# Kernel tuning notes

Hardware: AMD Instinct MI355X
Metric: run time of the kernel (lower is better)

## Reference

```python
import jax, jax.numpy as jnp
import numpy as np

N = 100_000      # nodes
E = 1_600_000    # edges (avg degree 16)
IN, HID, OUT = 256, 256, 128  # in_dim, 2*out_dim, out_dim
BN_EPS = 1e-5


def setup_inputs() -> dict:
    key = jax.random.key(0)
    ks = jax.random.split(key, 8)
    x = jax.random.normal(ks[0], (N, IN), jnp.float32)
    edge_index = jax.random.randint(ks[1], (2, E), 0, N, dtype=jnp.int64)
    # GCNConv weights (glorot-ish scaling) + biases
    W1 = jax.random.normal(ks[2], (IN, HID), jnp.float32) * (1.0 / np.sqrt(IN))
    b1 = jnp.zeros((HID,), jnp.float32)
    W2 = jax.random.normal(ks[3], (HID, OUT), jnp.float32) * (1.0 / np.sqrt(HID))
    b2 = jnp.zeros((OUT,), jnp.float32)
    # BatchNorm1d affine params
    gamma = jnp.ones((HID,), jnp.float32)
    beta = jnp.zeros((HID,), jnp.float32)
    # PReLU single learnable slope (torch default 0.25)
    a = jnp.full((1,), 0.25, jnp.float32)
    return {"x": x, "edge_index": edge_index, "W1": W1, "b1": b1,
            "W2": W2, "b2": b2, "gamma": gamma, "beta": beta, "a": a}


def gcn_layer(x, W, b, src, dst):
    """GCNConv: h = D^-1/2 (A + I) D^-1/2 (x @ W) + b, self-loop weight 1."""
    h = x @ W                                           # [N, F]
    deg = jnp.zeros((N,), h.dtype).at[dst].add(1.0) + 1.0  # +1 self-loop
    dinv = jax.lax.rsqrt(deg)                           # [N]
    norm = dinv[src] * dinv[dst]                        # [E]
    agg = jnp.zeros_like(h).at[dst].add(h[src] * norm[:, None])
    agg = agg + h * (dinv * dinv)[:, None]              # self-loop term
    return agg + b


def reference(x, edge_index, W1, b1, W2, b2, gamma, beta, a):
    src, dst = edge_index[0], edge_index[1]
    h = gcn_layer(x, W1, b1, src, dst)                  # [N, HID]
    # BatchNorm1d (training mode: batch statistics, biased var)
    mean = jnp.mean(h, axis=0)
    var = jnp.var(h, axis=0)
    h = (h - mean) * jax.lax.rsqrt(var + BN_EPS) * gamma + beta
    # PReLU with single shared slope
    h = jnp.where(h > 0, h, a * h)
    return gcn_layer(h, W2, b2, src, dst)               # [N, OUT]
```

## Files before the change

kernel.cpp:

```cpp
#include <hip/hip_runtime.h>
#include <hip/hip_bf16.h>
#include <stdint.h>

#define IN_DIM 256

typedef __attribute__((ext_vector_type(8))) short short8;
typedef __attribute__((ext_vector_type(4))) float f32x4;

__device__ __forceinline__ float bf2f(unsigned short u){
  return __uint_as_float(((unsigned int)u) << 16);
}
__device__ __forceinline__ unsigned short f2bf(float f){
  unsigned int u = __float_as_uint(f);
  u = u + 0x7FFFu + ((u >> 16) & 1u);
  return (unsigned short)(u >> 16);
}

__global__ void k_detect(const void* ei, long long E, int N, int* flag){
  __shared__ int bad;
  if (threadIdx.x == 0) bad = 0;
  __syncthreads();
  const long long* p = (const long long*)ei;
  long long stride = E / 1024; if (stride < 1) stride = 1;
  for (int i = threadIdx.x; i < 1024; i += blockDim.x){
    long long idx = (long long)i * stride;
    if (idx >= E) break;
    long long v = p[idx];
    if (v < 0 || v >= (long long)N) atomicOr(&bad, 1);
  }
  __syncthreads();
  if (threadIdx.x == 0) flag[0] = bad ? 0 : 1;
}

__device__ __forceinline__ int edge_at(const void* ei, long long i, int f64){
  if (f64) return (int)((const long long*)ei)[i];
  return ((const int*)ei)[i];
}

__global__ void k_hist(const void* ei, long long E, const int* flag, int* cnt){
  long long e = (long long)blockIdx.x * blockDim.x + threadIdx.x;
  if (e < E){
    int f = flag[0];
    int d = edge_at(ei, E + e, f);
    atomicAdd(&cnt[d], 1);
  }
}

__global__ void k_scan1(const int* cnt, int* rs, int* bsum, float* dinv, int* fill, int N){
  __shared__ int sh[1024];
  int i = blockIdx.x * 1024 + threadIdx.x;
  int v = (i < N) ? cnt[i] : 0;
  sh[threadIdx.x] = v;
  __syncthreads();
  for (int o = 1; o < 1024; o <<= 1){
    int x = (threadIdx.x >= o) ? sh[threadIdx.x - o] : 0;
    __syncthreads();
    sh[threadIdx.x] += x;
    __syncthreads();
  }
  if (i < N){
    rs[i] = sh[threadIdx.x] - v;
    dinv[i] = rsqrtf((float)v + 1.0f);
    fill[i] = 0;
  }
  if (threadIdx.x == 1023) bsum[blockIdx.x] = sh[1023];
}

__global__ void k_scan2(const int* bsum, int* boff, int nb, int* rs, int N,
                        float* sums, float* sqs){
  __shared__ int sh[128];
  int t = threadIdx.x;
  int v = (t < nb) ? bsum[t] : 0;
  sh[t] = v;
  __syncthreads();
  for (int o = 1; o < 128; o <<= 1){
    int x = (t >= o) ? sh[t - o] : 0;
    __syncthreads();
    sh[t] += x;
    __syncthreads();
  }
  boff[t] = sh[t] - v;
  if (t == 127) rs[N] = sh[127];
  sums[t] = 0.f; sums[t + 128] = 0.f;
  sqs[t]  = 0.f; sqs[t + 128]  = 0.f;
}

__global__ void k_scan3(int* rs, const int* boff, int N){
  int i = blockIdx.x * 1024 + threadIdx.x;
  if (i < N) rs[i] += boff[blockIdx.x];
}

__global__ void k_scatter(const void* ei, long long E, const int* flag, const int* rs,
                          int* fill, int* csrc){
  long long e = (long long)blockIdx.x * blockDim.x + threadIdx.x;
  if (e < E){
    int f = flag[0];
    int s = edge_at(ei, e, f);
    int d = edge_at(ei, E + e, f);
    int pos = atomicAdd(&fill[d], 1);
    csrc[rs[d] + pos] = s;
  }
}

__global__ void k_prep(const float* __restrict__ x, ushort* __restrict__ xb,
                       const float* __restrict__ W1, ushort* __restrict__ W1t,
                       const float* __restrict__ W2, ushort* __restrict__ W2t,
                       int N, int NP){
  int idx = blockIdx.x * 256 + threadIdx.x;
  int nxq = NP * 64;
  if (idx < nxq){
    int row = idx >> 6, q = idx & 63;
    ushort4 o = {0, 0, 0, 0};
    if (row < N){
      float4 v = ((const float4*)x)[(size_t)row * 64 + q];
      o.x = f2bf(v.x); o.y = f2bf(v.y); o.z = f2bf(v.z); o.w = f2bf(v.w);
    }
    ((ushort4*)xb)[idx] = o;
  } else {
    int j = idx - nxq;
    if (j < 256 * 256){
      int n = j >> 8, k = j & 255;
      W1t[j] = f2bf(W1[(size_t)k * 256 + n]);
    } else {
      j -= 65536;
      if (j < 128 * 256){
        int n = j >> 8, k = j & 255;
        W2t[j] = f2bf(W2[(size_t)k * 128 + n]);
      }
    }
  }
}

__global__ __launch_bounds__(256) void k_gemm(const ushort* __restrict__ A,
                                              const ushort* __restrict__ Bt,
                                              ushort* __restrict__ C,
                                              const float* __restrict__ dinv,
                                              int N, int Nc){
  __shared__ ushort As[128 * 64];
  __shared__ ushort Bs[128 * 64];
  const int tid = threadIdx.x;
  const int wave = tid >> 6, lane = tid & 63;
  const long long row0 = (long long)blockIdx.x * 128;
  const int col0 = blockIdx.y * 128;
  const int lr = lane >> 3, lc = lane & 7;
  const int mrow = ((wave & 1) << 6) + (lane & 15);
  const int ncol = ((wave >> 1) << 6) + (lane & 15);

  f32x4 acc[4][4];
  #pragma unroll
  for (int i = 0; i < 4; ++i)
    #pragma unroll
    for (int j = 0; j < 4; ++j)
      acc[i][j] = (f32x4){0.f, 0.f, 0.f, 0.f};

  const ushort* gA = A + (row0 + wave * 32 + lr) * 256 + lc * 8;
  const ushort* gB = Bt + ((long long)(col0 + wave * 32 + lr)) * 256 + lc * 8;
  ushort* lA = As + wave * 2048;
  ushort* lB = Bs + wave * 2048;

  #pragma unroll
  for (int kt = 0; kt < 4; ++kt){
    #pragma unroll
    for (int i = 0; i < 4; ++i){
      __builtin_amdgcn_global_load_lds(
          (const __attribute__((address_space(1))) void*)(gA + kt * 64 + i * 8 * 256),
          (__attribute__((address_space(3))) void*)(lA + i * 512), 16, 0, 0);
      __builtin_amdgcn_global_load_lds(
          (const __attribute__((address_space(1))) void*)(gB + kt * 64 + i * 8 * 256),
          (__attribute__((address_space(3))) void*)(lB + i * 512), 16, 0, 0);
    }
    __syncthreads();
    #pragma unroll
    for (int ks = 0; ks < 2; ++ks){
      const int kb = ks * 32 + ((lane >> 4) << 3);
      short8 af[4], bfv[4];
      #pragma unroll
      for (int i = 0; i < 4; ++i) af[i] = *(const short8*)(As + (mrow + i * 16) * 64 + kb);
      #pragma unroll
      for (int j = 0; j < 4; ++j) bfv[j] = *(const short8*)(Bs + (ncol + j * 16) * 64 + kb);
      #pragma unroll
      for (int i = 0; i < 4; ++i)
        #pragma unroll
        for (int j = 0; j < 4; ++j)
          acc[i][j] = __builtin_amdgcn_mfma_f32_16x16x32_bf16(af[i], bfv[j], acc[i][j], 0, 0, 0);
    }
    __syncthreads();
  }

  const int rbase = ((wave & 1) << 6) + ((lane >> 4) << 2);
  const int cb = col0 + ((wave >> 1) << 6) + (lane & 15);
  #pragma unroll
  for (int i = 0; i < 4; ++i)
    #pragma unroll
    for (int r = 0; r < 4; ++r){
      long long row = row0 + rbase + i * 16 + r;
      float sc = (row < N) ? dinv[row] : 0.f;
      #pragma unroll
      for (int j = 0; j < 4; ++j)
        C[row * Nc + cb + j * 16] = f2bf(sc * acc[i][j][r]);
    }
}

__global__ __launch_bounds__(64) void k_agg1(const ushort* __restrict__ hs, const int* __restrict__ rs,
    const int* __restrict__ csrc, const float* __restrict__ dinv, const float* __restrict__ b1,
    ushort* __restrict__ h1){
  int n = blockIdx.x;
  int t = threadIdx.x;
  const ushort4* hv = (const ushort4*)hs;
  ushort4 sv = hv[(size_t)n * 64 + t];
  float a0 = bf2f(sv.x), a1 = bf2f(sv.y), a2 = bf2f(sv.z), a3 = bf2f(sv.w);
  int e = rs[n], end = rs[n + 1];
  for (; e + 4 <= end; e += 4){
    int s0 = csrc[e], s1 = csrc[e + 1], s2 = csrc[e + 2], s3 = csrc[e + 3];
    ushort4 v0 = hv[(size_t)s0 * 64 + t];
    ushort4 v1 = hv[(size_t)s1 * 64 + t];
    ushort4 v2 = hv[(size_t)s2 * 64 + t];
    ushort4 v3 = hv[(size_t)s3 * 64 + t];
    a0 += bf2f(v0.x) + bf2f(v1.x) + bf2f(v2.x) + bf2f(v3.x);
    a1 += bf2f(v0.y) + bf2f(v1.y) + bf2f(v2.y) + bf2f(v3.y);
    a2 += bf2f(v0.z) + bf2f(v1.z) + bf2f(v2.z) + bf2f(v3.z);
    a3 += bf2f(v0.w) + bf2f(v1.w) + bf2f(v2.w) + bf2f(v3.w);
  }
  for (; e < end; ++e){
    int s = csrc[e];
    ushort4 v = hv[(size_t)s * 64 + t];
    a0 += bf2f(v.x); a1 += bf2f(v.y); a2 += bf2f(v.z); a3 += bf2f(v.w);
  }
  float dn = dinv[n];
  float4 bb = ((const float4*)b1)[t];
  ushort4 o;
  o.x = f2bf(dn * a0 + bb.x);
  o.y = f2bf(dn * a1 + bb.y);
  o.z = f2bf(dn * a2 + bb.z);
  o.w = f2bf(dn * a3 + bb.w);
  ((ushort4*)h1)[(size_t)n * 64 + t] = o;
}

__global__ __launch_bounds__(64) void k_agg2(const ushort* __restrict__ h2, const int* __restrict__ rs,
    const int* __restrict__ csrc, const float* __restrict__ dinv, const float* __restrict__ b2,
    float* __restrict__ out){
  int n = blockIdx.x;
  int t = threadIdx.x;
  const uint* hv = (const uint*)h2;
  uint sv = hv[(size_t)n * 64 + t];
  float a0 = bf2f((unsigned short)(sv & 0xFFFF));
  float a1 = bf2f((unsigned short)(sv >> 16));
  int e = rs[n], end = rs[n + 1];
  for (; e + 4 <= end; e += 4){
    int s0 = csrc[e], s1 = csrc[e + 1], s2 = csrc[e + 2], s3 = csrc[e + 3];
    uint v0 = hv[(size_t)s0 * 64 + t];
    uint v1 = hv[(size_t)s1 * 64 + t];
    uint v2 = hv[(size_t)s2 * 64 + t];
    uint v3 = hv[(size_t)s3 * 64 + t];
    a0 += bf2f((unsigned short)(v0 & 0xFFFF)) + bf2f((unsigned short)(v1 & 0xFFFF))
        + bf2f((unsigned short)(v2 & 0xFFFF)) + bf2f((unsigned short)(v3 & 0xFFFF));
    a1 += bf2f((unsigned short)(v0 >> 16)) + bf2f((unsigned short)(v1 >> 16))
        + bf2f((unsigned short)(v2 >> 16)) + bf2f((unsigned short)(v3 >> 16));
  }
  for (; e < end; ++e){
    int s = csrc[e];
    uint v = hv[(size_t)s * 64 + t];
    a0 += bf2f((unsigned short)(v & 0xFFFF));
    a1 += bf2f((unsigned short)(v >> 16));
  }
  float dn = dinv[n];
  float2 bb = ((const float2*)b2)[t];
  float2 r; r.x = dn * a0 + bb.x; r.y = dn * a1 + bb.y;
  ((float2*)out)[(size_t)n * 64 + t] = r;
}

__global__ void k_bnstats(const ushort* __restrict__ h1, float* __restrict__ sums,
                          float* __restrict__ sqs, int N){
  int cp = threadIdx.x & 127, ro = threadIdx.x >> 7;
  const uint* hv = (const uint*)h1;
  float s0 = 0.f, s1 = 0.f, q0 = 0.f, q1 = 0.f;
  for (int r = blockIdx.x * 2 + ro; r < N; r += gridDim.x * 2){
    uint v = hv[(size_t)r * 128 + cp];
    float x0 = bf2f((unsigned short)(v & 0xFFFF));
    float x1 = bf2f((unsigned short)(v >> 16));
    s0 += x0; q0 += x0 * x0;
    s1 += x1; q1 += x1 * x1;
  }
  atomicAdd(&sums[2 * cp],     s0);
  atomicAdd(&sums[2 * cp + 1], s1);
  atomicAdd(&sqs[2 * cp],      q0);
  atomicAdd(&sqs[2 * cp + 1],  q1);
}

__global__ void k_prelu(const ushort* __restrict__ h1, const float* __restrict__ sums,
                        const float* __restrict__ sqs, const float* __restrict__ gamma,
                        const float* __restrict__ beta, const float* __restrict__ aP,
                        ushort* __restrict__ P, int N, int NP){
  int idx = blockIdx.x * 256 + threadIdx.x;
  int row = idx >> 7, cp = idx & 127;
  if (row >= NP) return;
  uint o = 0;
  if (row < N){
    int c0 = 2 * cp;
    float inv = 1.0f / (float)N;
    float m0 = sums[c0] * inv,     m1 = sums[c0 + 1] * inv;
    float v0 = sqs[c0] * inv - m0 * m0, v1 = sqs[c0 + 1] * inv - m1 * m1;
    float sc0 = gamma[c0] * rsqrtf(v0 + 1e-5f);
    float sc1 = gamma[c0 + 1] * rsqrtf(v1 + 1e-5f);
    float sh0 = beta[c0] - m0 * sc0;
    float sh1 = beta[c0 + 1] - m1 * sc1;
    uint v = ((const uint*)h1)[(size_t)row * 128 + cp];
    float aa = aP[0];
    float x0 = bf2f((unsigned short)(v & 0xFFFF)) * sc0 + sh0;
    float x1 = bf2f((unsigned short)(v >> 16)) * sc1 + sh1;
    x0 = x0 > 0.f ? x0 : aa * x0;
    x1 = x1 > 0.f ? x1 : aa * x1;
    o = (uint)f2bf(x0) | ((uint)f2bf(x1) << 16);
  }
  ((uint*)P)[idx] = o;
}

extern "C" void kernel_launch(void* const* d_in, const int* in_sizes, int n_in,
                              void* d_out, int out_size, void* d_ws, size_t ws_size,
                              hipStream_t stream){
  const float* x  = (const float*)d_in[0];
  const void*  ei = d_in[1];
  const float* W1 = (const float*)d_in[2];
  const float* b1 = (const float*)d_in[3];
  const float* W2 = (const float*)d_in[4];
  const float* b2 = (const float*)d_in[5];
  const float* gm = (const float*)d_in[6];
  const float* bt = (const float*)d_in[7];
  const float* aP = (const float*)d_in[8];
  float* out = (float*)d_out;

  const int N = in_sizes[0] / IN_DIM;
  const long long E = in_sizes[1] / 2;
  const int NP = ((N + 127) / 128) * 128;

  char* w = (char*)d_ws;
  size_t off = 0;
  auto carve = [&](size_t bytes) -> char* {
    char* p = w + off;
    off += (bytes + 255) & ~(size_t)255;
    return p;
  };
  ushort* xb  = (ushort*)carve((size_t)NP * 256 * 2);
  ushort* hb  = (ushort*)carve((size_t)NP * 256 * 2);
  ushort* h1b = (ushort*)carve((size_t)NP * 256 * 2);
  ushort* W1t = (ushort*)carve(256 * 256 * 2);
  ushort* W2t = (ushort*)carve(128 * 256 * 2);
  int*   cnt  = (int*)  carve((size_t)N * 4);
  int*   rs   = (int*)  carve((size_t)(N + 1) * 4);
  int*   fill = (int*)  carve((size_t)N * 4);
  int*   csrc = (int*)  carve((size_t)E * 4);
  float* dinv = (float*)carve((size_t)N * 4);
  int*   bsum = (int*)  carve(512);
  int*   boff = (int*)  carve(512);
  float* sums = (float*)carve(1024);
  float* sqs  = (float*)carve(1024);
  int*   flag = (int*)  carve(256);

  const int NB1 = (N + 1023) / 1024;
  const int egrid = (int)((E + 255) / 256);
  const int prep_grid = (NP * 64 + 256 * 256 + 128 * 256 + 255) / 256;

  k_detect<<<1, 256, 0, stream>>>(ei, E, N, flag);
  hipMemsetAsync(cnt, 0, (size_t)N * 4, stream);
  k_prep<<<prep_grid, 256, 0, stream>>>(x, xb, W1, W1t, W2, W2t, N, NP);
  k_hist<<<egrid, 256, 0, stream>>>(ei, E, flag, cnt);
  k_scan1<<<NB1, 1024, 0, stream>>>(cnt, rs, bsum, dinv, fill, N);
  k_scan2<<<1, 128, 0, stream>>>(bsum, boff, NB1, rs, N, sums, sqs);
  k_scan3<<<NB1, 1024, 0, stream>>>(rs, boff, N);
  k_scatter<<<egrid, 256, 0, stream>>>(ei, E, flag, rs, fill, csrc);

  k_gemm<<<dim3(NP / 128, 2), 256, 0, stream>>>(xb, W1t, hb, dinv, N, 256);
  k_agg1<<<N, 64, 0, stream>>>(hb, rs, csrc, dinv, b1, h1b);
  k_bnstats<<<256, 256, 0, stream>>>(h1b, sums, sqs, N);
  k_prelu<<<(NP * 128 + 255) / 256, 256, 0, stream>>>(h1b, sums, sqs, gm, bt, aP, xb, N, NP);
  k_gemm<<<dim3(NP / 128, 1), 256, 0, stream>>>(xb, W2t, hb, dinv, N, 128);
  k_agg2<<<N, 64, 0, stream>>>(hb, rs, csrc, dinv, b2, out);
}
```

Baseline: 675.5 us.

## Use persistent wave-per-node aggregation with wave-wide index load and readlane broadcast

Both aggregation kernels switch from one 64-thread block per node to a fixed grid of 2048 blocks of 256 threads. Each wave walks nodes in a grid-stride loop. A wave loads up to 64 neighbour indices in one coalesced read, broadcasts them with readlane, and unrolls the gathers by 8 to keep more loads in flight. This removes the cost of launching 100k tiny blocks and the scalar per-edge index loads. In exchange, the fixed grid may leave load imbalance across waves when node degrees vary.

```diff
diff --git a/kernel.cpp b/kernel.cpp
--- a/kernel.cpp
+++ b/kernel.cpp
@@ -3,6 +3,7 @@
 #include <stdint.h>
 
 #define IN_DIM 256
+#define AGG_BLOCKS 2048
 
 typedef __attribute__((ext_vector_type(8))) short short8;
 typedef __attribute__((ext_vector_type(4))) float f32x4;
@@ -201,72 +202,123 @@
     }
 }
 
-__global__ __launch_bounds__(64) void k_agg1(const ushort* __restrict__ hs, const int* __restrict__ rs,
+__global__ __launch_bounds__(256) void k_agg1(const ushort* __restrict__ hs, const int* __restrict__ rs,
     const int* __restrict__ csrc, const float* __restrict__ dinv, const float* __restrict__ b1,
-    ushort* __restrict__ h1){
-  int n = blockIdx.x;
-  int t = threadIdx.x;
-  const ushort4* hv = (const ushort4*)hs;
-  ushort4 sv = hv[(size_t)n * 64 + t];
-  float a0 = bf2f(sv.x), a1 = bf2f(sv.y), a2 = bf2f(sv.z), a3 = bf2f(sv.w);
-  int e = rs[n], end = rs[n + 1];
-  for (; e + 4 <= end; e += 4){
-    int s0 = csrc[e], s1 = csrc[e + 1], s2 = csrc[e + 2], s3 = csrc[e + 3];
-    ushort4 v0 = hv[(size_t)s0 * 64 + t];
-    ushort4 v1 = hv[(size_t)s1 * 64 + t];
-    ushort4 v2 = hv[(size_t)s2 * 64 + t];
-    ushort4 v3 = hv[(size_t)s3 * 64 + t];
-    a0 += bf2f(v0.x) + bf2f(v1.x) + bf2f(v2.x) + bf2f(v3.x);
-    a1 += bf2f(v0.y) + bf2f(v1.y) + bf2f(v2.y) + bf2f(v3.y);
-    a2 += bf2f(v0.z) + bf2f(v1.z) + bf2f(v2.z) + bf2f(v3.z);
-    a3 += bf2f(v0.w) + bf2f(v1.w) + bf2f(v2.w) + bf2f(v3.w);
-  }
-  for (; e < end; ++e){
-    int s = csrc[e];
-    ushort4 v = hv[(size_t)s * 64 + t];
-    a0 += bf2f(v.x); a1 += bf2f(v.y); a2 += bf2f(v.z); a3 += bf2f(v.w);
-  }
-  float dn = dinv[n];
-  float4 bb = ((const float4*)b1)[t];
-  ushort4 o;
-  o.x = f2bf(dn * a0 + bb.x);
-  o.y = f2bf(dn * a1 + bb.y);
-  o.z = f2bf(dn * a2 + bb.z);
-  o.w = f2bf(dn * a3 + bb.w);
-  ((ushort4*)h1)[(size_t)n * 64 + t] = o;
-}
-
-__global__ __launch_bounds__(64) void k_agg2(const ushort* __restrict__ h2, const int* __restrict__ rs,
+    ushort* __restrict__ h1, int N){
+  const int lane = threadIdx.x & 63;
+  const int wid = (blockIdx.x * 256 + threadIdx.x) >> 6;
+  const int nw = (AGG_BLOCKS * 256) >> 6;
+  const float4 bb = ((const float4*)b1)[lane];
+
+  for (int n = wid; n < N; n += nw){
+    const ushort4* selfp = (const ushort4*)(hs + (size_t)n * 256);
+    ushort4 sv = selfp[lane];
+    float a0 = bf2f(sv.x), a1 = bf2f(sv.y), a2 = bf2f(sv.z), a3 = bf2f(sv.w);
+    int e0 = rs[n], deg = rs[n + 1] - e0;
+
+    for (int c = 0; c < deg; c += 64){
+      int chunk = deg - c; if (chunk > 64) chunk = 64;
+      int myc = 0;
+      if (lane < chunk) myc = csrc[e0 + c + lane];
+      int j = 0;
+      for (; j + 8 <= chunk; j += 8){
+        int s0 = __builtin_amdgcn_readlane(myc, j);
+        int s1 = __builtin_amdgcn_readlane(myc, j + 1);
+        int s2 = __builtin_amdgcn_readlane(myc, j + 2);
+        int s3 = __builtin_amdgcn_readlane(myc, j + 3);
+        int s4 = __builtin_amdgcn_readlane(myc, j + 4);
+        int s5 = __builtin_amdgcn_readlane(myc, j + 5);
+        int s6 = __builtin_amdgcn_readlane(myc, j + 6);
+        int s7 = __builtin_amdgcn_readlane(myc, j + 7);
+        ushort4 v0 = ((const ushort4*)(hs + (size_t)s0 * 256))[lane];
+        ushort4 v1 = ((const ushort4*)(hs + (size_t)s1 * 256))[lane];
+        ushort4 v2 = ((const ushort4*)(hs + (size_t)s2 * 256))[lane];
+        ushort4 v3 = ((const ushort4*)(hs + (size_t)s3 * 256))[lane];
+        ushort4 v4 = ((const ushort4*)(hs + (size_t)s4 * 256))[lane];
+        ushort4 v5 = ((const ushort4*)(hs + (size_t)s5 * 256))[lane];
+        ushort4 v6 = ((const ushort4*)(hs + (size_t)s6 * 256))[lane];
+        ushort4 v7 = ((const ushort4*)(hs + (size_t)s7 * 256))[lane];
+        a0 += ((bf2f(v0.x) + bf2f(v1.x)) + (bf2f(v2.x) + bf2f(v3.x)))
+            + ((bf2f(v4.x) + bf2f(v5.x)) + (bf2f(v6.x) + bf2f(v7.x)));
+        a1 += ((bf2f(v0.y) + bf2f(v1.y)) + (bf2f(v2.y) + bf2f(v3.y)))
+            + ((bf2f(v4.y) + bf2f(v5.y)) + (bf2f(v6.y) + bf2f(v7.y)));
+        a2 += ((bf2f(v0.z) + bf2f(v1.z)) + (bf2f(v2.z) + bf2f(v3.z)))
+            + ((bf2f(v4.z) + bf2f(v5.z)) + (bf2f(v6.z) + bf2f(v7.z)));
+        a3 += ((bf2f(v0.w) + bf2f(v1.w)) + (bf2f(v2.w) + bf2f(v3.w)))
+            + ((bf2f(v4.w) + bf2f(v5.w)) + (bf2f(v6.w) + bf2f(v7.w)));
+      }
+      for (; j < chunk; ++j){
+        int s = __builtin_amdgcn_readlane(myc, j);
+        ushort4 v = ((const ushort4*)(hs + (size_t)s * 256))[lane];
+        a0 += bf2f(v.x); a1 += bf2f(v.y); a2 += bf2f(v.z); a3 += bf2f(v.w);
+      }
+    }
+    float dn = dinv[n];
+    ushort4 o;
+    o.x = f2bf(dn * a0 + bb.x);
+    o.y = f2bf(dn * a1 + bb.y);
+    o.z = f2bf(dn * a2 + bb.z);
+    o.w = f2bf(dn * a3 + bb.w);
+    ((ushort4*)h1)[(size_t)n * 64 + lane] = o;
+  }
+}
+
+__global__ __launch_bounds__(256) void k_agg2(const ushort* __restrict__ h2, const int* __restrict__ rs,
     const int* __restrict__ csrc, const float* __restrict__ dinv, const float* __restrict__ b2,
-    float* __restrict__ out){
-  int n = blockIdx.x;
-  int t = threadIdx.x;
-  const uint* hv = (const uint*)h2;
-  uint sv = hv[(size_t)n * 64 + t];
-  float a0 = bf2f((unsigned short)(sv & 0xFFFF));
-  float a1 = bf2f((unsigned short)(sv >> 16));
-  int e = rs[n], end = rs[n + 1];
-  for (; e + 4 <= end; e += 4){
-    int s0 = csrc[e], s1 = csrc[e + 1], s2 = csrc[e + 2], s3 = csrc[e + 3];
-    uint v0 = hv[(size_t)s0 * 64 + t];
-    uint v1 = hv[(size_t)s1 * 64 + t];
-    uint v2 = hv[(size_t)s2 * 64 + t];
-    uint v3 = hv[(size_t)s3 * 64 + t];
-    a0 += bf2f((unsigned short)(v0 & 0xFFFF)) + bf2f((unsigned short)(v1 & 0xFFFF))
-        + bf2f((unsigned short)(v2 & 0xFFFF)) + bf2f((unsigned short)(v3 & 0xFFFF));
-    a1 += bf2f((unsigned short)(v0 >> 16)) + bf2f((unsigned short)(v1 >> 16))
-        + bf2f((unsigned short)(v2 >> 16)) + bf2f((unsigned short)(v3 >> 16));
-  }
-  for (; e < end; ++e){
-    int s = csrc[e];
-    uint v = hv[(size_t)s * 64 + t];
-    a0 += bf2f((unsigned short)(v & 0xFFFF));
-    a1 += bf2f((unsigned short)(v >> 16));
-  }
-  float dn = dinv[n];
-  float2 bb = ((const float2*)b2)[t];
-  float2 r; r.x = dn * a0 + bb.x; r.y = dn * a1 + bb.y;
-  ((float2*)out)[(size_t)n * 64 + t] = r;
+    float* __restrict__ out, int N){
+  const int lane = threadIdx.x & 63;
+  const int wid = (blockIdx.x * 256 + threadIdx.x) >> 6;
+  const int nw = (AGG_BLOCKS * 256) >> 6;
+  const float2 bb = ((const float2*)b2)[lane];
+
+  for (int n = wid; n < N; n += nw){
+    uint sv = ((const uint*)(h2 + (size_t)n * 128))[lane];
+    float a0 = bf2f((unsigned short)(sv & 0xFFFF));
+    float a1 = bf2f((unsigned short)(sv >> 16));
+    int e0 = rs[n], deg = rs[n + 1] - e0;
+
+    for (int c = 0; c < deg; c += 64){
+      int chunk = deg - c; if (chunk > 64) chunk = 64;
+      int myc = 0;
+      if (lane < chunk) myc = csrc[e0 + c + lane];
+      int j = 0;
+      for (; j + 8 <= chunk; j += 8){
+        int s0 = __builtin_amdgcn_readlane(myc, j);
+        int s1 = __builtin_amdgcn_readlane(myc, j + 1);
+        int s2 = __builtin_amdgcn_readlane(myc, j + 2);
+        int s3 = __builtin_amdgcn_readlane(myc, j + 3);
+        int s4 = __builtin_amdgcn_readlane(myc, j + 4);
+        int s5 = __builtin_amdgcn_readlane(myc, j + 5);
+        int s6 = __builtin_amdgcn_readlane(myc, j + 6);
+        int s7 = __builtin_amdgcn_readlane(myc, j + 7);
+        uint v0 = ((const uint*)(h2 + (size_t)s0 * 128))[lane];
+        uint v1 = ((const uint*)(h2 + (size_t)s1 * 128))[lane];
+        uint v2 = ((const uint*)(h2 + (size_t)s2 * 128))[lane];
+        uint v3 = ((const uint*)(h2 + (size_t)s3 * 128))[lane];
+        uint v4 = ((const uint*)(h2 + (size_t)s4 * 128))[lane];
+        uint v5 = ((const uint*)(h2 + (size_t)s5 * 128))[lane];
+        uint v6 = ((const uint*)(h2 + (size_t)s6 * 128))[lane];
+        uint v7 = ((const uint*)(h2 + (size_t)s7 * 128))[lane];
+        a0 += ((bf2f((unsigned short)(v0 & 0xFFFF)) + bf2f((unsigned short)(v1 & 0xFFFF)))
+             + (bf2f((unsigned short)(v2 & 0xFFFF)) + bf2f((unsigned short)(v3 & 0xFFFF))))
+            + ((bf2f((unsigned short)(v4 & 0xFFFF)) + bf2f((unsigned short)(v5 & 0xFFFF)))
+             + (bf2f((unsigned short)(v6 & 0xFFFF)) + bf2f((unsigned short)(v7 & 0xFFFF))));
+        a1 += ((bf2f((unsigned short)(v0 >> 16)) + bf2f((unsigned short)(v1 >> 16)))
+             + (bf2f((unsigned short)(v2 >> 16)) + bf2f((unsigned short)(v3 >> 16))))
+            + ((bf2f((unsigned short)(v4 >> 16)) + bf2f((unsigned short)(v5 >> 16)))
+             + (bf2f((unsigned short)(v6 >> 16)) + bf2f((unsigned short)(v7 >> 16))));
+      }
+      for (; j < chunk; ++j){
+        int s = __builtin_amdgcn_readlane(myc, j);
+        uint v = ((const uint*)(h2 + (size_t)s * 128))[lane];
+        a0 += bf2f((unsigned short)(v & 0xFFFF));
+        a1 += bf2f((unsigned short)(v >> 16));
+      }
+    }
+    float dn = dinv[n];
+    float2 r; r.x = dn * a0 + bb.x; r.y = dn * a1 + bb.y;
+    ((float2*)out)[(size_t)n * 64 + lane] = r;
+  }
 }
 
 __global__ void k_bnstats(const ushort* __restrict__ h1, float* __restrict__ sums,
@@ -370,9 +422,9 @@
   k_scatter<<<egrid, 256, 0, stream>>>(ei, E, flag, rs, fill, csrc);
 
   k_gemm<<<dim3(NP / 128, 2), 256, 0, stream>>>(xb, W1t, hb, dinv, N, 256);
-  k_agg1<<<N, 64, 0, stream>>>(hb, rs, csrc, dinv, b1, h1b);
+  k_agg1<<<AGG_BLOCKS, 256, 0, stream>>>(hb, rs, csrc, dinv, b1, h1b, N);
   k_bnstats<<<256, 256, 0, stream>>>(h1b, sums, sqs, N);
   k_prelu<<<(NP * 128 + 255) / 256, 256, 0, stream>>>(h1b, sums, sqs, gm, bt, aP, xb, N, NP);
   k_gemm<<<dim3(NP / 128, 1), 256, 0, stream>>>(xb, W2t, hb, dinv, N, 128);
-  k_agg2<<<N, 64, 0, stream>>>(hb, rs, csrc, dinv, b2, out);
-}
+  k_agg2<<<AGG_BLOCKS, 256, 0, stream>>>(hb, rs, csrc, dinv, b2, out, N);
+}
```

After: 684.5 us. Within noise of the previous version (+1.3%).

## Quantize features to per-row int8 before gather and fuse BN stats into aggregation

Applied to the files above, without the earlier changes.

Adds quantization kernels that turn each bf16 row of the GEMM output into uint8 codes plus one per-row float scale. Both aggregation kernels then gather these half-size rows and undo the quantization with a per-neighbour scale sum and a -128 offset correction. The kernels become grid-strided persistent waves that recompute dinv from the row pointers. The first aggregation also accumulates the BatchNorm sums and sums of squares, which removes the separate stats pass. The goal is to halve gather bandwidth, at the cost of two extra quantize passes and lower numerical precision.

```diff
diff --git a/kernel.cpp b/kernel.cpp
--- a/kernel.cpp
+++ b/kernel.cpp
@@ -15,6 +15,18 @@
   u = u + 0x7FFFu + ((u >> 16) & 1u);
   return (unsigned short)(u >> 16);
 }
+
+#if __has_builtin(__builtin_amdgcn_cvt_f32_ubyte0)
+__device__ __forceinline__ float ub0(uint v){ return __builtin_amdgcn_cvt_f32_ubyte0(v); }
+__device__ __forceinline__ float ub1(uint v){ return __builtin_amdgcn_cvt_f32_ubyte1(v); }
+__device__ __forceinline__ float ub2(uint v){ return __builtin_amdgcn_cvt_f32_ubyte2(v); }
+__device__ __forceinline__ float ub3(uint v){ return __builtin_amdgcn_cvt_f32_ubyte3(v); }
+#else
+__device__ __forceinline__ float ub0(uint v){ return (float)(v & 0xFF); }
+__device__ __forceinline__ float ub1(uint v){ return (float)((v >> 8) & 0xFF); }
+__device__ __forceinline__ float ub2(uint v){ return (float)((v >> 16) & 0xFF); }
+__device__ __forceinline__ float ub3(uint v){ return (float)(v >> 24); }
+#endif
 
 __global__ void k_detect(const void* ei, long long E, int N, int* flag){
   __shared__ int bad;
@@ -201,90 +213,154 @@
     }
 }
 
-__global__ __launch_bounds__(64) void k_agg1(const ushort* __restrict__ hs, const int* __restrict__ rs,
-    const int* __restrict__ csrc, const float* __restrict__ dinv, const float* __restrict__ b1,
-    ushort* __restrict__ h1){
-  int n = blockIdx.x;
-  int t = threadIdx.x;
-  const ushort4* hv = (const ushort4*)hs;
-  ushort4 sv = hv[(size_t)n * 64 + t];
-  float a0 = bf2f(sv.x), a1 = bf2f(sv.y), a2 = bf2f(sv.z), a3 = bf2f(sv.w);
-  int e = rs[n], end = rs[n + 1];
-  for (; e + 4 <= end; e += 4){
-    int s0 = csrc[e], s1 = csrc[e + 1], s2 = csrc[e + 2], s3 = csrc[e + 3];
-    ushort4 v0 = hv[(size_t)s0 * 64 + t];
-    ushort4 v1 = hv[(size_t)s1 * 64 + t];
-    ushort4 v2 = hv[(size_t)s2 * 64 + t];
-    ushort4 v3 = hv[(size_t)s3 * 64 + t];
-    a0 += bf2f(v0.x) + bf2f(v1.x) + bf2f(v2.x) + bf2f(v3.x);
-    a1 += bf2f(v0.y) + bf2f(v1.y) + bf2f(v2.y) + bf2f(v3.y);
-    a2 += bf2f(v0.z) + bf2f(v1.z) + bf2f(v2.z) + bf2f(v3.z);
-    a3 += bf2f(v0.w) + bf2f(v1.w) + bf2f(v2.w) + bf2f(v3.w);
-  }
-  for (; e < end; ++e){
-    int s = csrc[e];
-    ushort4 v = hv[(size_t)s * 64 + t];
-    a0 += bf2f(v.x); a1 += bf2f(v.y); a2 += bf2f(v.z); a3 += bf2f(v.w);
-  }
-  float dn = dinv[n];
-  float4 bb = ((const float4*)b1)[t];
-  ushort4 o;
-  o.x = f2bf(dn * a0 + bb.x);
-  o.y = f2bf(dn * a1 + bb.y);
-  o.z = f2bf(dn * a2 + bb.z);
-  o.w = f2bf(dn * a3 + bb.w);
-  ((ushort4*)h1)[(size_t)n * 64 + t] = o;
-}
-
-__global__ __launch_bounds__(64) void k_agg2(const ushort* __restrict__ h2, const int* __restrict__ rs,
-    const int* __restrict__ csrc, const float* __restrict__ dinv, const float* __restrict__ b2,
-    float* __restrict__ out){
-  int n = blockIdx.x;
-  int t = threadIdx.x;
-  const uint* hv = (const uint*)h2;
-  uint sv = hv[(size_t)n * 64 + t];
-  float a0 = bf2f((unsigned short)(sv & 0xFFFF));
-  float a1 = bf2f((unsigned short)(sv >> 16));
-  int e = rs[n], end = rs[n + 1];
-  for (; e + 4 <= end; e += 4){
-    int s0 = csrc[e], s1 = csrc[e + 1], s2 = csrc[e + 2], s3 = csrc[e + 3];
-    uint v0 = hv[(size_t)s0 * 64 + t];
-    uint v1 = hv[(size_t)s1 * 64 + t];
-    uint v2 = hv[(size_t)s2 * 64 + t];
-    uint v3 = hv[(size_t)s3 * 64 + t];
-    a0 += bf2f((unsigned short)(v0 & 0xFFFF)) + bf2f((unsigned short)(v1 & 0xFFFF))
-        + bf2f((unsigned short)(v2 & 0xFFFF)) + bf2f((unsigned short)(v3 & 0xFFFF));
-    a1 += bf2f((unsigned short)(v0 >> 16)) + bf2f((unsigned short)(v1 >> 16))
-        + bf2f((unsigned short)(v2 >> 16)) + bf2f((unsigned short)(v3 >> 16));
-  }
-  for (; e < end; ++e){
-    int s = csrc[e];
-    uint v = hv[(size_t)s * 64 + t];
-    a0 += bf2f((unsigned short)(v & 0xFFFF));
-    a1 += bf2f((unsigned short)(v >> 16));
-  }
-  float dn = dinv[n];
-  float2 bb = ((const float2*)b2)[t];
-  float2 r; r.x = dn * a0 + bb.x; r.y = dn * a1 + bb.y;
-  ((float2*)out)[(size_t)n * 64 + t] = r;
-}
-
-__global__ void k_bnstats(const ushort* __restrict__ h1, float* __restrict__ sums,
-                          float* __restrict__ sqs, int N){
-  int cp = threadIdx.x & 127, ro = threadIdx.x >> 7;
-  const uint* hv = (const uint*)h1;
-  float s0 = 0.f, s1 = 0.f, q0 = 0.f, q1 = 0.f;
-  for (int r = blockIdx.x * 2 + ro; r < N; r += gridDim.x * 2){
-    uint v = hv[(size_t)r * 128 + cp];
-    float x0 = bf2f((unsigned short)(v & 0xFFFF));
-    float x1 = bf2f((unsigned short)(v >> 16));
-    s0 += x0; q0 += x0 * x0;
-    s1 += x1; q1 += x1 * x1;
-  }
-  atomicAdd(&sums[2 * cp],     s0);
-  atomicAdd(&sums[2 * cp + 1], s1);
-  atomicAdd(&sqs[2 * cp],      q0);
-  atomicAdd(&sqs[2 * cp + 1],  q1);
+__global__ __launch_bounds__(256) void k_quant1(const ushort* __restrict__ hb,
+    uint* __restrict__ q, float* __restrict__ sc, int N){
+  int lane = threadIdx.x & 63;
+  int r = blockIdx.x * 4 + (threadIdx.x >> 6);
+  if (r >= N) return;
+  ushort4 v = ((const ushort4*)hb)[(size_t)r * 64 + lane];
+  float f0 = bf2f(v.x), f1 = bf2f(v.y), f2 = bf2f(v.z), f3 = bf2f(v.w);
+  float m = fmaxf(fmaxf(fabsf(f0), fabsf(f1)), fmaxf(fabsf(f2), fabsf(f3)));
+  #pragma unroll
+  for (int o = 32; o >= 1; o >>= 1) m = fmaxf(m, __shfl_xor(m, o, 64));
+  float scale = m * (1.0f / 127.0f);
+  float inv = (m > 0.f) ? 127.0f / m : 0.f;
+  uint b0 = (uint)(int)(rintf(f0 * inv) + 128.0f);
+  uint b1 = (uint)(int)(rintf(f1 * inv) + 128.0f);
+  uint b2 = (uint)(int)(rintf(f2 * inv) + 128.0f);
+  uint b3 = (uint)(int)(rintf(f3 * inv) + 128.0f);
+  q[(size_t)r * 64 + lane] = b0 | (b1 << 8) | (b2 << 16) | (b3 << 24);
+  if (lane == 0) sc[r] = scale;
+}
+
+__global__ __launch_bounds__(256) void k_quant2(const ushort* __restrict__ hb,
+    ushort* __restrict__ q, float* __restrict__ sc, int N){
+  int lane = threadIdx.x & 63;
+  int r = blockIdx.x * 4 + (threadIdx.x >> 6);
+  if (r >= N) return;
+  uint v = ((const uint*)hb)[(size_t)r * 64 + lane];
+  float f0 = bf2f((unsigned short)(v & 0xFFFF));
+  float f1 = bf2f((unsigned short)(v >> 16));
+  float m = fmaxf(fabsf(f0), fabsf(f1));
+  #pragma unroll
+  for (int o = 32; o >= 1; o >>= 1) m = fmaxf(m, __shfl_xor(m, o, 64));
+  float scale = m * (1.0f / 127.0f);
+  float inv = (m > 0.f) ? 127.0f / m : 0.f;
+  uint b0 = (uint)(int)(rintf(f0 * inv) + 128.0f);
+  uint b1 = (uint)(int)(rintf(f1 * inv) + 128.0f);
+  q[(size_t)r * 64 + lane] = (ushort)(b0 | (b1 << 8));
+  if (lane == 0) sc[r] = scale;
+}
+
+__global__ __launch_bounds__(256) void k_agg1(const uint* __restrict__ q, const float* __restrict__ sc,
+    const int* __restrict__ rs, const int* __restrict__ csrc, const float* __restrict__ b1,
+    ushort* __restrict__ h1, float* __restrict__ sums, float* __restrict__ sqs,
+    int N, int nblocks){
+  __shared__ float red[4 * 512];
+  const int lane = threadIdx.x & 63;
+  const int wid = (blockIdx.x * 256 + threadIdx.x) >> 6;
+  const int nw = (nblocks * 256) >> 6;
+  const float4 bb = ((const float4*)b1)[lane];
+  float st0 = 0.f, st1 = 0.f, st2 = 0.f, st3 = 0.f;
+  float sq0 = 0.f, sq1 = 0.f, sq2 = 0.f, sq3 = 0.f;
+
+  for (int n = wid; n < N; n += nw){
+    int e = rs[n], end = rs[n + 1];
+    float dn = rsqrtf((float)(end - e) + 1.0f);
+    float scn = sc[n];
+    uint v = q[(size_t)n * 64 + lane];
+    float ssum = scn;
+    float a0 = scn * ub0(v), a1 = scn * ub1(v), a2 = scn * ub2(v), a3 = scn * ub3(v);
+    for (; e + 4 <= end; e += 4){
+      int s0 = csrc[e], s1 = csrc[e + 1], s2 = csrc[e + 2], s3 = csrc[e + 3];
+      float c0 = sc[s0], c1 = sc[s1], c2 = sc[s2], c3 = sc[s3];
+      uint v0 = q[(size_t)s0 * 64 + lane];
+      uint v1 = q[(size_t)s1 * 64 + lane];
+      uint v2 = q[(size_t)s2 * 64 + lane];
+      uint v3 = q[(size_t)s3 * 64 + lane];
+      ssum += (c0 + c1) + (c2 + c3);
+      a0 += (c0 * ub0(v0) + c1 * ub0(v1)) + (c2 * ub0(v2) + c3 * ub0(v3));
+      a1 += (c0 * ub1(v0) + c1 * ub1(v1)) + (c2 * ub1(v2) + c3 * ub1(v3));
+      a2 += (c0 * ub2(v0) + c1 * ub2(v1)) + (c2 * ub2(v2) + c3 * ub2(v3));
+      a3 += (c0 * ub3(v0) + c1 * ub3(v1)) + (c2 * ub3(v2) + c3 * ub3(v3));
+    }
+    for (; e < end; ++e){
+      int s = csrc[e];
+      float c = sc[s];
+      uint vv = q[(size_t)s * 64 + lane];
+      ssum += c;
+      a0 += c * ub0(vv); a1 += c * ub1(vv); a2 += c * ub2(vv); a3 += c * ub3(vv);
+    }
+    float corr = -128.0f * ssum;
+    float h0 = dn * (a0 + corr) + bb.x;
+    float h1v = dn * (a1 + corr) + bb.y;
+    float h2 = dn * (a2 + corr) + bb.z;
+    float h3 = dn * (a3 + corr) + bb.w;
+    st0 += h0; st1 += h1v; st2 += h2; st3 += h3;
+    sq0 += h0 * h0; sq1 += h1v * h1v; sq2 += h2 * h2; sq3 += h3 * h3;
+    ushort4 o;
+    o.x = f2bf(h0); o.y = f2bf(h1v); o.z = f2bf(h2); o.w = f2bf(h3);
+    ((ushort4*)h1)[(size_t)n * 64 + lane] = o;
+  }
+
+  int wv = threadIdx.x >> 6;
+  int f = lane * 4;
+  red[wv * 512 + f]     = st0; red[wv * 512 + f + 1] = st1;
+  red[wv * 512 + f + 2] = st2; red[wv * 512 + f + 3] = st3;
+  __syncthreads();
+  float v0s = red[threadIdx.x] + red[512 + threadIdx.x] + red[1024 + threadIdx.x] + red[1536 + threadIdx.x];
+  float v1s = (threadIdx.x < 256) ? 0.f : 0.f;
+  __syncthreads();
+  red[wv * 512 + f]     = sq0; red[wv * 512 + f + 1] = sq1;
+  red[wv * 512 + f + 2] = sq2; red[wv * 512 + f + 3] = sq3;
+  __syncthreads();
+  float v0q = red[threadIdx.x] + red[512 + threadIdx.x] + red[1024 + threadIdx.x] + red[1536 + threadIdx.x];
+  (void)v1s;
+  if (threadIdx.x < 256){
+    atomicAdd(&sums[threadIdx.x], v0s);
+    atomicAdd(&sqs[threadIdx.x], v0q);
+  }
+}
+
+__global__ __launch_bounds__(256) void k_agg2(const ushort* __restrict__ q, const float* __restrict__ sc,
+    const int* __restrict__ rs, const int* __restrict__ csrc, const float* __restrict__ b2,
+    float* __restrict__ out, int N, int nblocks){
+  const int lane = threadIdx.x & 63;
+  const int wid = (blockIdx.x * 256 + threadIdx.x) >> 6;
+  const int nw = (nblocks * 256) >> 6;
+  const float2 bb = ((const float2*)b2)[lane];
+
+  for (int n = wid; n < N; n += nw){
+    int e = rs[n], end = rs[n + 1];
+    float dn = rsqrtf((float)(end - e) + 1.0f);
+    float scn = sc[n];
+    uint v = (uint)q[(size_t)n * 64 + lane];
+    float ssum = scn;
+    float a0 = scn * ub0(v), a1 = scn * ub1(v);
+    for (; e + 4 <= end; e += 4){
+      int s0 = csrc[e], s1 = csrc[e + 1], s2 = csrc[e + 2], s3 = csrc[e + 3];
+      float c0 = sc[s0], c1 = sc[s1], c2 = sc[s2], c3 = sc[s3];
+      uint v0 = (uint)q[(size_t)s0 * 64 + lane];
+      uint v1 = (uint)q[(size_t)s1 * 64 + lane];
+      uint v2 = (uint)q[(size_t)s2 * 64 + lane];
+      uint v3 = (uint)q[(size_t)s3 * 64 + lane];
+      ssum += (c0 + c1) + (c2 + c3);
+      a0 += (c0 * ub0(v0) + c1 * ub0(v1)) + (c2 * ub0(v2) + c3 * ub0(v3));
+      a1 += (c0 * ub1(v0) + c1 * ub1(v1)) + (c2 * ub1(v2) + c3 * ub1(v3));
+    }
+    for (; e < end; ++e){
+      int s = csrc[e];
+      float c = sc[s];
+      uint vv = (uint)q[(size_t)s * 64 + lane];
+      ssum += c;
+      a0 += c * ub0(vv); a1 += c * ub1(vv);
+    }
+    float corr = -128.0f * ssum;
+    float2 r;
+    r.x = dn * (a0 + corr) + bb.x;
+    r.y = dn * (a1 + corr) + bb.y;
+    ((float2*)out)[(size_t)n * 64 + lane] = r;
+  }
 }
 
 __global__ void k_prelu(const ushort* __restrict__ h1, const float* __restrict__ sums,
@@ -350,15 +426,20 @@
   int*   fill = (int*)  carve((size_t)N * 4);
   int*   csrc = (int*)  carve((size_t)E * 4);
   float* dinv = (float*)carve((size_t)N * 4);
+  float* sc1  = (float*)carve((size_t)N * 4);
+  float* sc2  = (float*)carve((size_t)N * 4);
   int*   bsum = (int*)  carve(512);
   int*   boff = (int*)  carve(512);
   float* sums = (float*)carve(1024);
   float* sqs  = (float*)carve(1024);
   int*   flag = (int*)  carve(256);
+  uint*   q8a = (uint*)xb;
+  ushort* q8b = (ushort*)h1b;
 
   const int NB1 = (N + 1023) / 1024;
   const int egrid = (int)((E + 255) / 256);
   const int prep_grid = (NP * 64 + 256 * 256 + 128 * 256 + 255) / 256;
+  const int AGG1_BLOCKS = 1024, AGG2_BLOCKS = 2048;
 
   k_detect<<<1, 256, 0, stream>>>(ei, E, N, flag);
   hipMemsetAsync(cnt, 0, (size_t)N * 4, stream);
@@ -370,9 +451,10 @@
   k_scatter<<<egrid, 256, 0, stream>>>(ei, E, flag, rs, fill, csrc);
 
   k_gemm<<<dim3(NP / 128, 2), 256, 0, stream>>>(xb, W1t, hb, dinv, N, 256);
-  k_agg1<<<N, 64, 0, stream>>>(hb, rs, csrc, dinv, b1, h1b);
-  k_bnstats<<<256, 256, 0, stream>>>(h1b, sums, sqs, N);
+  k_quant1<<<(N + 3) / 4, 256, 0, stream>>>(hb, q8a, sc1, N);
+  k_agg1<<<AGG1_BLOCKS, 256, 0, stream>>>(q8a, sc1, rs, csrc, b1, h1b, sums, sqs, N, AGG1_BLOCKS);
   k_prelu<<<(NP * 128 + 255) / 256, 256, 0, stream>>>(h1b, sums, sqs, gm, bt, aP, xb, N, NP);
   k_gemm<<<dim3(NP / 128, 1), 256, 0, stream>>>(xb, W2t, hb, dinv, N, 128);
-  k_agg2<<<N, 64, 0, stream>>>(hb, rs, csrc, dinv, b2, out);
-}
+  k_quant2<<<(N + 3) / 4, 256, 0, stream>>>(hb, q8b, sc2, N);
+  k_agg2<<<AGG2_BLOCKS, 256, 0, stream>>>(q8b, sc2, rs, csrc, b2, out, N, AGG2_BLOCKS);
+}
```

Result: faster. 638.5 us (-5.5%).
